# Optimization experiments

Measured on AMD Instinct MI355X. Metric: run time of the kernel, lower is better.

## Reference

```python
import jax, jax.numpy as jnp
import numpy as np

N_AGENTS = 512
HID = 256
OBS = 128


def setup_inputs() -> dict:
    key = jax.random.key(0)
    ks = jax.random.split(key, 10)
    s = 0.02  # weight init scale
    f32 = jnp.float32
    return {
        "inputs": jax.random.normal(ks[0], (N_AGENTS, OBS), f32),
        "fc1_w": jax.random.normal(ks[1], (HID, OBS), f32) * s,
        "fc1_b": jnp.zeros((HID,), f32),
        "in_proj_w": jax.random.normal(ks[2], (3 * HID, HID), f32) * s,
        "in_proj_b": jnp.zeros((3 * HID,), f32),
        "out_proj_w": jax.random.normal(ks[3], (HID, HID), f32) * s,
        "out_proj_b": jnp.zeros((HID,), f32),
        "fc2_w": jax.random.normal(ks[4], (HID, 2 * HID), f32) * s,
        "fc2_b": jnp.zeros((HID,), f32),
        "fc3_w": jax.random.normal(ks[5], (2, HID), f32) * s,
        "fc3_b": jnp.zeros((2,), f32),
        "vfc2_w": jax.random.normal(ks[6], (HID, HID * N_AGENTS), f32) * s,
        "vfc2_b": jnp.zeros((HID,), f32),
        "vfc3_w": jax.random.normal(ks[7], (1, HID), f32) * s,
        "vfc3_b": jnp.zeros((1,), f32),
    }


def reference(inputs, fc1_w, fc1_b, in_proj_w, in_proj_b, out_proj_w, out_proj_b,
              fc2_w, fc2_b, fc3_w, fc3_b, vfc2_w, vfc2_b, vfc3_w, vfc3_b):
    n = inputs.shape[0]
    d = fc1_w.shape[0]
    # per-agent embed
    hid = jax.nn.relu(inputs @ fc1_w.T + fc1_b)                 # [n, d]
    # single-head self-attention (torch MultiheadAttention, 1 head)
    qkv = hid @ in_proj_w.T + in_proj_b                         # [n, 3d]
    q, k, v = jnp.split(qkv, 3, axis=-1)
    scores = (q @ k.T) / jnp.sqrt(jnp.asarray(d, hid.dtype))    # [n, n]
    attn = jax.nn.softmax(scores, axis=-1)
    h = (attn @ v) @ out_proj_w.T + out_proj_b                  # [n, d]
    # all-pairs edge features restricted to strict upper triangle
    iu0, iu1 = jnp.triu_indices(n, 1)                           # P = n(n-1)/2
    pairs = jnp.concatenate([h[iu0], h[iu1]], axis=1)           # [P, 2d]
    x = jax.nn.relu(pairs @ fc2_w.T + fc2_b)                    # [P, d]
    action_out = jax.nn.softmax(x @ fc3_w.T + fc3_b, axis=-1)   # [P, 2]
    # value head over flattened node embeddings
    vh = jax.nn.relu(hid.reshape(1, -1) @ vfc2_w.T + vfc2_b)    # [1, d]
    value = vh @ vfc3_w.T + vfc3_b                              # [1, 1]
    value = jnp.broadcast_to(value, (action_out.shape[0], 1))   # [P, 1]
    return jnp.concatenate([action_out, value], axis=1)         # [P, 3]
```

## Files before the change

### kernel.cpp

```cpp
#include <hip/hip_runtime.h>
#include <math.h>

#define N_AG   512
#define HIDD   256
#define OBSD   128

__device__ __forceinline__ void fma4(float4& acc, float4 a, float4 b){
    acc.x += a.x*b.x; acc.y += a.y*b.y; acc.z += a.z*b.z; acc.w += a.w*b.w;
}
__device__ __forceinline__ float hsum(float4 a){ return (a.x+a.y)+(a.z+a.w); }

__device__ __forceinline__ void stage_rows(float* dst, const float* __restrict__ src,
        int row0, int stride, int colbase, int t){
    #pragma unroll
    for (int half = 0; half < 2; ++half){
        int idx = half*256 + t;
        int row = idx >> 3, c4 = idx & 7;
        float4 v = *(const float4*)(src + (row0+row)*stride + colbase + c4*4);
        dst[(c4*4+0)*68 + row] = v.x;
        dst[(c4*4+1)*68 + row] = v.y;
        dst[(c4*4+2)*68 + row] = v.z;
        dst[(c4*4+3)*68 + row] = v.w;
    }
}
__device__ __forceinline__ void tile_compute(const float* As, const float* Bs,
        int tx, int ty, float4 acc[4]){
    #pragma unroll
    for (int kk = 0; kk < 32; ++kk){
        float4 a = *(const float4*)(As + kk*68 + ty*4);
        float4 b = *(const float4*)(Bs + kk*68 + tx*4);
        acc[0].x += a.x*b.x; acc[0].y += a.x*b.y; acc[0].z += a.x*b.z; acc[0].w += a.x*b.w;
        acc[1].x += a.y*b.x; acc[1].y += a.y*b.y; acc[1].z += a.y*b.z; acc[1].w += a.y*b.w;
        acc[2].x += a.z*b.x; acc[2].y += a.z*b.y; acc[2].z += a.z*b.z; acc[2].w += a.z*b.w;
        acc[3].x += a.w*b.x; acc[3].y += a.w*b.y; acc[3].z += a.w*b.z; acc[3].w += a.w*b.w;
    }
}

__global__ __launch_bounds__(256, 2) void k_fc1(const float* __restrict__ in,
        const float* __restrict__ w, const float* __restrict__ b,
        float* __restrict__ hid){
    __shared__ float lin[8*OBSD];
    int at = blockIdx.y, ot = blockIdx.x, t = threadIdx.x;
    ((float4*)lin)[t] = ((const float4*)(in + at*8*OBSD))[t];
    __syncthreads();
    int ol = t & 63, g = t >> 6;
    int o = ot*64 + ol;
    const float4* w4 = (const float4*)(w + o*OBSD);
    const float4* la = (const float4*)(lin + (g*2)*OBSD);
    const float4* lb = (const float4*)(lin + (g*2+1)*OBSD);
    float4 a0 = {0,0,0,0}, a1 = {0,0,0,0};
    #pragma unroll
    for (int c = 0; c < OBSD/4; ++c){
        float4 wv = w4[c];
        fma4(a0, la[c], wv);
        fma4(a1, lb[c], wv);
    }
    float bb = b[o];
    int ag = at*8 + g*2;
    hid[ag*HIDD + o]     = fmaxf(hsum(a0) + bb, 0.f);
    hid[(ag+1)*HIDD + o] = fmaxf(hsum(a1) + bb, 0.f);
}

__global__ __launch_bounds__(256, 2) void k_qkv(const float* __restrict__ hid,
        const float* __restrict__ w, const float* __restrict__ b,
        float* __restrict__ qkv){
    __shared__ float lin[8*HIDD];
    int at = blockIdx.y, ot = blockIdx.x, t = threadIdx.x;
    const float4* in4 = (const float4*)(hid + at*8*HIDD);
    ((float4*)lin)[t]       = in4[t];
    ((float4*)lin)[t + 256] = in4[t + 256];
    __syncthreads();
    int ol = t & 63, g = t >> 6;
    int o = ot*64 + ol;
    const float4* w4 = (const float4*)(w + o*HIDD);
    const float4* la = (const float4*)(lin + (g*2)*HIDD);
    const float4* lb = (const float4*)(lin + (g*2+1)*HIDD);
    float4 a0 = {0,0,0,0}, a1 = {0,0,0,0};
    #pragma unroll 8
    for (int c = 0; c < HIDD/4; ++c){
        float4 wv = w4[c];
        fma4(a0, la[c], wv);
        fma4(a1, lb[c], wv);
    }
    float bb = b[o];
    int ag = at*8 + g*2;
    qkv[ag*768 + o]     = hsum(a0) + bb;
    qkv[(ag+1)*768 + o] = hsum(a1) + bb;
}

__global__ __launch_bounds__(256, 2) void k_big(const float* __restrict__ qkv,
        const float* __restrict__ ow, const float* __restrict__ hid,
        const float* __restrict__ vw_w, float* __restrict__ S,
        float* __restrict__ VW, float* __restrict__ partial){
    __shared__ float As[32*68];
    __shared__ float Bs[32*68];
    int t = threadIdx.x;
    int bid = blockIdx.x;
    if (bid < 64){
        int ti = bid >> 3, tj = bid & 7;
        int i0 = ti*64, j0 = tj*64;
        int tx = t & 15, ty = t >> 4;
        float4 acc[4] = {{0,0,0,0},{0,0,0,0},{0,0,0,0},{0,0,0,0}};
        for (int k0 = 0; k0 < 256; k0 += 32){
            __syncthreads();
            stage_rows(As, qkv, i0, 768, k0,       t);
            stage_rows(Bs, qkv, j0, 768, 256 + k0, t);
            __syncthreads();
            tile_compute(As, Bs, tx, ty, acc);
        }
        #pragma unroll
        for (int r = 0; r < 4; ++r){
            float4 o;
            o.x = acc[r].x*0.0625f; o.y = acc[r].y*0.0625f;
            o.z = acc[r].z*0.0625f; o.w = acc[r].w*0.0625f;
            *(float4*)(S + (i0+ty*4+r)*512 + j0 + tx*4) = o;
        }
        return;
    }
    if (bid < 96){
        int b2 = bid - 64;
        int ti = b2 >> 2, tj = b2 & 3;
        int j0 = ti*64, d0 = tj*64;
        int tx = t & 15, ty = t >> 4;
        float4 acc[4] = {{0,0,0,0},{0,0,0,0},{0,0,0,0},{0,0,0,0}};
        for (int k0 = 0; k0 < 256; k0 += 32){
            __syncthreads();
            stage_rows(As, qkv, j0, 768, 512 + k0, t);
            stage_rows(Bs, ow,  d0, 256, k0,       t);
            __syncthreads();
            tile_compute(As, Bs, tx, ty, acc);
        }
        #pragma unroll
        for (int r = 0; r < 4; ++r)
            *(float4*)(VW + (j0+ty*4+r)*256 + d0 + tx*4) = acc[r];
        return;
    }
    int id = bid - 96;
    int chunk = id & 7, o = id >> 3;
    const float4* h4 = (const float4*)hid;
    const float4* w4 = (const float4*)vw_w;
    long base  = (long)chunk*4096;
    long wbase = (long)o*32768 + base;
    float4 aa = {0,0,0,0}, ab = {0,0,0,0};
    #pragma unroll 4
    for (int it = 0; it < 8; ++it){
        fma4(aa, h4[base + it*256 + t],     w4[wbase + it*256 + t]);
        fma4(ab, h4[base + (it+8)*256 + t], w4[wbase + (it+8)*256 + t]);
    }
    float acc = hsum(aa) + hsum(ab);
    for (int off = 32; off; off >>= 1) acc += __shfl_xor(acc, off);
    int lane = t & 63, wid = t >> 6;
    if (lane == 0) As[wid] = acc;
    __syncthreads();
    if (t == 0) partial[o*8 + chunk] = As[0]+As[1]+As[2]+As[3];
}

__global__ __launch_bounds__(256, 2) void k_softmax(float* __restrict__ S){
    int t = threadIdx.x, w = t >> 6, ln = t & 63;
    float* row = S + (blockIdx.x*4 + w)*512;
    float v[8];
    float m = -1e30f;
    #pragma unroll
    for (int k = 0; k < 8; ++k){ v[k] = row[ln + k*64]; m = fmaxf(m, v[k]); }
    for (int off = 32; off; off >>= 1) m = fmaxf(m, __shfl_xor(m, off));
    float s = 0.f;
    #pragma unroll
    for (int k = 0; k < 8; ++k){ v[k] = expf(v[k] - m); s += v[k]; }
    for (int off = 32; off; off >>= 1) s += __shfl_xor(s, off);
    float inv = 1.f / s;
    #pragma unroll
    for (int k = 0; k < 8; ++k) row[ln + k*64] = v[k]*inv;
}

__global__ __launch_bounds__(256, 2) void k_h(const float* __restrict__ P,
        const float* __restrict__ VW, const float* __restrict__ ob,
        float* __restrict__ hout){
    __shared__ float As[32*68];
    __shared__ float Bs[32*68];
    int bid = blockIdx.x;
    int ti = bid >> 2, tj = bid & 3;
    int i0 = ti*64, d0 = tj*64;
    int t = threadIdx.x, tx = t & 15, ty = t >> 4;
    float4 acc[4] = {{0,0,0,0},{0,0,0,0},{0,0,0,0},{0,0,0,0}};
    for (int k0 = 0; k0 < 512; k0 += 32){
        __syncthreads();
        stage_rows(As, P, i0, 512, k0, t);
        #pragma unroll
        for (int half = 0; half < 2; ++half){
            int idx = half*256 + t;
            int kkr = idx >> 4, c4 = idx & 15;
            *(float4*)(Bs + kkr*68 + c4*4) = *(const float4*)(VW + (k0+kkr)*256 + d0 + c4*4);
        }
        __syncthreads();
        tile_compute(As, Bs, tx, ty, acc);
    }
    float4 bb = *(const float4*)(ob + d0 + tx*4);
    #pragma unroll
    for (int r = 0; r < 4; ++r){
        float4 o;
        o.x = acc[r].x + bb.x; o.y = acc[r].y + bb.y;
        o.z = acc[r].z + bb.z; o.w = acc[r].w + bb.w;
        *(float4*)(hout + (i0+ty*4+r)*256 + d0 + tx*4) = o;
    }
}

__global__ __launch_bounds__(256, 2) void k_ab_value(const float* __restrict__ hin,
        const float* __restrict__ w2, const float* __restrict__ b2,
        const float* __restrict__ partial, const float* __restrict__ vb,
        const float* __restrict__ v3w, const float* __restrict__ v3b,
        float* __restrict__ A, float* __restrict__ B, float* __restrict__ value){
    int t = threadIdx.x;
    if (blockIdx.x == 512){
        float s = vb[t];
        #pragma unroll
        for (int c = 0; c < 8; ++c) s += partial[t*8 + c];
        s = fmaxf(s, 0.f) * v3w[t];
        for (int off = 32; off; off >>= 1) s += __shfl_xor(s, off);
        __shared__ float redv[4];
        int lane = t & 63, wid = t >> 6;
        if (lane == 0) redv[wid] = s;
        __syncthreads();
        if (t == 0) value[0] = redv[0]+redv[1]+redv[2]+redv[3] + v3b[0];
        return;
    }
    __shared__ float lin[8*HIDD];
    int id = blockIdx.x, at = id >> 3, ot = id & 7;
    const float4* in4 = (const float4*)(hin + at*8*HIDD);
    ((float4*)lin)[t]       = in4[t];
    ((float4*)lin)[t + 256] = in4[t + 256];
    __syncthreads();
    int ol = t & 63, g = t >> 6;
    int o2 = ot*64 + ol;
    bool isA = o2 < HIDD;
    int o = isA ? o2 : o2 - HIDD;
    const float4* w4 = (const float4*)(w2 + o*512 + (isA ? 0 : HIDD));
    const float4* la = (const float4*)(lin + (g*2)*HIDD);
    const float4* lb = (const float4*)(lin + (g*2+1)*HIDD);
    float4 acc0 = {0,0,0,0}, acc1 = {0,0,0,0};
    #pragma unroll 8
    for (int c = 0; c < HIDD/4; ++c){
        float4 wv = w4[c];
        fma4(acc0, la[c], wv);
        fma4(acc1, lb[c], wv);
    }
    int a0 = at*8 + g*2;
    float* dst = isA ? A : B;
    float bb = isA ? b2[o] : 0.f;
    dst[a0*HIDD + o]     = hsum(acc0) + bb;
    dst[(a0+1)*HIDD + o] = hsum(acc1) + bb;
}

__global__ __launch_bounds__(256, 2) void k_pairs(const float* __restrict__ A,
        const float* __restrict__ B, const float* __restrict__ w3,
        const float* __restrict__ b3, const float* __restrict__ value,
        float* __restrict__ out){
    int ti = blockIdx.x, tj = blockIdx.y;
    if (tj < ti) return;
    __shared__ float la[16*260], lb[16*260], lw[256];
    int t = threadIdx.x;
    #pragma unroll
    for (int l = 0; l < 4; ++l){
        int idx = l*256 + t;
        int r = idx >> 6, c4 = idx & 63;
        ((float4*)la)[r*65 + c4] = ((const float4*)A)[(ti*16 + r)*64 + c4];
        ((float4*)lb)[r*65 + c4] = ((const float4*)B)[(tj*16 + r)*64 + c4];
    }
    lw[t] = w3[t] - w3[256 + t];
    __syncthreads();
    float val = value[0];
    float bd  = b3[0] - b3[1];
    int il = t >> 4, jl = t & 15;
    int i = ti*16 + il, j = tj*16 + jl;
    if (j > i){
        const float4* a4 = (const float4*)(la + il*260);
        const float4* b4 = (const float4*)(lb + jl*260);
        const float4* w4 = (const float4*)lw;
        float4 acc = {0,0,0,0};
        #pragma unroll 8
        for (int c = 0; c < 64; ++c){
            float4 aa = a4[c], bb = b4[c], wv = w4[c];
            acc.x += fmaxf(aa.x + bb.x, 0.f)*wv.x;
            acc.y += fmaxf(aa.y + bb.y, 0.f)*wv.y;
            acc.z += fmaxf(aa.z + bb.z, 0.f)*wv.z;
            acc.w += fmaxf(aa.w + bb.w, 0.f)*wv.w;
        }
        float z = hsum(acc) + bd;
        float o0 = 1.f/(1.f + expf(-z));
        int p = i*511 - (i*(i-1))/2 + (j - i - 1);
        out[3*p]   = o0;
        out[3*p+1] = 1.f - o0;
        out[3*p+2] = val;
    }
}

extern "C" void kernel_launch(void* const* d_in, const int* in_sizes, int n_in,
                              void* d_out, int out_size, void* d_ws, size_t ws_size,
                              hipStream_t stream){
    const float* inputs = (const float*)d_in[0];
    const float* fc1_w  = (const float*)d_in[1];
    const float* fc1_b  = (const float*)d_in[2];
    const float* inp_w  = (const float*)d_in[3];
    const float* inp_b  = (const float*)d_in[4];
    const float* outp_w = (const float*)d_in[5];
    const float* outp_b = (const float*)d_in[6];
    const float* fc2_w  = (const float*)d_in[7];
    const float* fc2_b  = (const float*)d_in[8];
    const float* fc3_w  = (const float*)d_in[9];
    const float* fc3_b  = (const float*)d_in[10];
    const float* vfc2_w = (const float*)d_in[11];
    const float* vfc2_b = (const float*)d_in[12];
    const float* vfc3_w = (const float*)d_in[13];
    const float* vfc3_b = (const float*)d_in[14];
    float* out = (float*)d_out;
    float* ws  = (float*)d_ws;
    float* hid     = ws;
    float* qkv     = ws + 131072;
    float* S       = ws + 524288;
    float* VW      = ws + 786432;
    float* h       = ws + 917504;
    float* A       = ws + 1048576;
    float* B       = ws + 1179648;
    float* partial = ws + 1310720;
    float* value   = ws + 1312768;

    k_fc1     <<<dim3(4, 64),  256, 0, stream>>>(inputs, fc1_w, fc1_b, hid);
    k_qkv     <<<dim3(12, 64), 256, 0, stream>>>(hid, inp_w, inp_b, qkv);
    k_big     <<<dim3(2144),   256, 0, stream>>>(qkv, outp_w, hid, vfc2_w, S, VW, partial);
    k_softmax <<<dim3(128),    256, 0, stream>>>(S);
    k_h       <<<dim3(32),     256, 0, stream>>>(S, VW, outp_b, h);
    k_ab_value<<<dim3(513),    256, 0, stream>>>(h, fc2_w, fc2_b, partial, vfc2_b, vfc3_w, vfc3_b, A, B, value);
    k_pairs   <<<dim3(32, 32), 256, 0, stream>>>(A, B, fc3_w, fc3_b, value, out);
}
```

Before: 299.0 us.

## Fuse pipeline into persistent megakernel with software grid barriers

Replaces the seven kernel launches with one persistent 512-block kernel whose stages are separated by atomic grid barriers. The large value-head weight stream is split across two stages so it runs alongside the attention GEMMs. Softmax is folded into the attn@V tile load, and fc1 and qkv are fused per agent group. The aim is to remove launch gaps and idle tails between small kernels, at the cost of barrier spin overhead and relying on all 512 blocks being co-resident for the barrier to avoid deadlock.

```diff
diff --git a/kernel.cpp b/kernel.cpp
--- a/kernel.cpp
+++ b/kernel.cpp
@@ -5,10 +5,30 @@
 #define HIDD   256
 #define OBSD   128
 
+#define NBLK   512u
+
 __device__ __forceinline__ void fma4(float4& acc, float4 a, float4 b){
     acc.x += a.x*b.x; acc.y += a.y*b.y; acc.z += a.z*b.z; acc.w += a.w*b.w;
 }
 __device__ __forceinline__ float hsum(float4 a){ return (a.x+a.y)+(a.z+a.w); }
+
+__device__ __forceinline__ void grid_barrier(unsigned* bar, unsigned* gen){
+    __threadfence();
+    __syncthreads();
+    if (threadIdx.x == 0){
+        unsigned g = __hip_atomic_load(gen, __ATOMIC_RELAXED, __HIP_MEMORY_SCOPE_AGENT);
+        unsigned a = __hip_atomic_fetch_add(bar, 1u, __ATOMIC_ACQ_REL, __HIP_MEMORY_SCOPE_AGENT) + 1u;
+        if (a == NBLK){
+            __hip_atomic_store(bar, 0u, __ATOMIC_RELAXED, __HIP_MEMORY_SCOPE_AGENT);
+            __hip_atomic_fetch_add(gen, 1u, __ATOMIC_RELEASE, __HIP_MEMORY_SCOPE_AGENT);
+        } else {
+            while (__hip_atomic_load(gen, __ATOMIC_ACQUIRE, __HIP_MEMORY_SCOPE_AGENT) == g)
+                __builtin_amdgcn_s_sleep(1);
+        }
+    }
+    __syncthreads();
+    __threadfence();
+}
 
 __device__ __forceinline__ void stage_rows(float* dst, const float* __restrict__ src,
         int row0, int stride, int colbase, int t){
@@ -36,109 +56,12 @@
     }
 }
 
-__global__ __launch_bounds__(256, 2) void k_fc1(const float* __restrict__ in,
-        const float* __restrict__ w, const float* __restrict__ b,
-        float* __restrict__ hid){
-    __shared__ float lin[8*OBSD];
-    int at = blockIdx.y, ot = blockIdx.x, t = threadIdx.x;
-    ((float4*)lin)[t] = ((const float4*)(in + at*8*OBSD))[t];
-    __syncthreads();
-    int ol = t & 63, g = t >> 6;
-    int o = ot*64 + ol;
-    const float4* w4 = (const float4*)(w + o*OBSD);
-    const float4* la = (const float4*)(lin + (g*2)*OBSD);
-    const float4* lb = (const float4*)(lin + (g*2+1)*OBSD);
-    float4 a0 = {0,0,0,0}, a1 = {0,0,0,0};
-    #pragma unroll
-    for (int c = 0; c < OBSD/4; ++c){
-        float4 wv = w4[c];
-        fma4(a0, la[c], wv);
-        fma4(a1, lb[c], wv);
-    }
-    float bb = b[o];
-    int ag = at*8 + g*2;
-    hid[ag*HIDD + o]     = fmaxf(hsum(a0) + bb, 0.f);
-    hid[(ag+1)*HIDD + o] = fmaxf(hsum(a1) + bb, 0.f);
-}
-
-__global__ __launch_bounds__(256, 2) void k_qkv(const float* __restrict__ hid,
-        const float* __restrict__ w, const float* __restrict__ b,
-        float* __restrict__ qkv){
-    __shared__ float lin[8*HIDD];
-    int at = blockIdx.y, ot = blockIdx.x, t = threadIdx.x;
-    const float4* in4 = (const float4*)(hid + at*8*HIDD);
-    ((float4*)lin)[t]       = in4[t];
-    ((float4*)lin)[t + 256] = in4[t + 256];
-    __syncthreads();
-    int ol = t & 63, g = t >> 6;
-    int o = ot*64 + ol;
-    const float4* w4 = (const float4*)(w + o*HIDD);
-    const float4* la = (const float4*)(lin + (g*2)*HIDD);
-    const float4* lb = (const float4*)(lin + (g*2+1)*HIDD);
-    float4 a0 = {0,0,0,0}, a1 = {0,0,0,0};
-    #pragma unroll 8
-    for (int c = 0; c < HIDD/4; ++c){
-        float4 wv = w4[c];
-        fma4(a0, la[c], wv);
-        fma4(a1, lb[c], wv);
-    }
-    float bb = b[o];
-    int ag = at*8 + g*2;
-    qkv[ag*768 + o]     = hsum(a0) + bb;
-    qkv[(ag+1)*768 + o] = hsum(a1) + bb;
-}
-
-__global__ __launch_bounds__(256, 2) void k_big(const float* __restrict__ qkv,
-        const float* __restrict__ ow, const float* __restrict__ hid,
-        const float* __restrict__ vw_w, float* __restrict__ S,
-        float* __restrict__ VW, float* __restrict__ partial){
-    __shared__ float As[32*68];
-    __shared__ float Bs[32*68];
-    int t = threadIdx.x;
-    int bid = blockIdx.x;
-    if (bid < 64){
-        int ti = bid >> 3, tj = bid & 7;
-        int i0 = ti*64, j0 = tj*64;
-        int tx = t & 15, ty = t >> 4;
-        float4 acc[4] = {{0,0,0,0},{0,0,0,0},{0,0,0,0},{0,0,0,0}};
-        for (int k0 = 0; k0 < 256; k0 += 32){
-            __syncthreads();
-            stage_rows(As, qkv, i0, 768, k0,       t);
-            stage_rows(Bs, qkv, j0, 768, 256 + k0, t);
-            __syncthreads();
-            tile_compute(As, Bs, tx, ty, acc);
-        }
-        #pragma unroll
-        for (int r = 0; r < 4; ++r){
-            float4 o;
-            o.x = acc[r].x*0.0625f; o.y = acc[r].y*0.0625f;
-            o.z = acc[r].z*0.0625f; o.w = acc[r].w*0.0625f;
-            *(float4*)(S + (i0+ty*4+r)*512 + j0 + tx*4) = o;
-        }
-        return;
-    }
-    if (bid < 96){
-        int b2 = bid - 64;
-        int ti = b2 >> 2, tj = b2 & 3;
-        int j0 = ti*64, d0 = tj*64;
-        int tx = t & 15, ty = t >> 4;
-        float4 acc[4] = {{0,0,0,0},{0,0,0,0},{0,0,0,0},{0,0,0,0}};
-        for (int k0 = 0; k0 < 256; k0 += 32){
-            __syncthreads();
-            stage_rows(As, qkv, j0, 768, 512 + k0, t);
-            stage_rows(Bs, ow,  d0, 256, k0,       t);
-            __syncthreads();
-            tile_compute(As, Bs, tx, ty, acc);
-        }
-        #pragma unroll
-        for (int r = 0; r < 4; ++r)
-            *(float4*)(VW + (j0+ty*4+r)*256 + d0 + tx*4) = acc[r];
-        return;
-    }
-    int id = bid - 96;
-    int chunk = id & 7, o = id >> 3;
+__device__ __forceinline__ void stream_unit(int u, const float* __restrict__ hid,
+        const float* __restrict__ vw2, float* __restrict__ partial,
+        float* red, int t){
+    int chunk = u & 7, o = u >> 3;
     const float4* h4 = (const float4*)hid;
-    const float4* w4 = (const float4*)vw_w;
+    const float4* w4 = (const float4*)vw2;
     long base  = (long)chunk*4096;
     long wbase = (long)o*32768 + base;
     float4 aa = {0,0,0,0}, ab = {0,0,0,0};
@@ -150,146 +73,276 @@
     float acc = hsum(aa) + hsum(ab);
     for (int off = 32; off; off >>= 1) acc += __shfl_xor(acc, off);
     int lane = t & 63, wid = t >> 6;
-    if (lane == 0) As[wid] = acc;
+    if (lane == 0) red[wid] = acc;
     __syncthreads();
-    if (t == 0) partial[o*8 + chunk] = As[0]+As[1]+As[2]+As[3];
-}
-
-__global__ __launch_bounds__(256, 2) void k_softmax(float* __restrict__ S){
-    int t = threadIdx.x, w = t >> 6, ln = t & 63;
-    float* row = S + (blockIdx.x*4 + w)*512;
-    float v[8];
-    float m = -1e30f;
-    #pragma unroll
-    for (int k = 0; k < 8; ++k){ v[k] = row[ln + k*64]; m = fmaxf(m, v[k]); }
-    for (int off = 32; off; off >>= 1) m = fmaxf(m, __shfl_xor(m, off));
-    float s = 0.f;
-    #pragma unroll
-    for (int k = 0; k < 8; ++k){ v[k] = expf(v[k] - m); s += v[k]; }
-    for (int off = 32; off; off >>= 1) s += __shfl_xor(s, off);
-    float inv = 1.f / s;
-    #pragma unroll
-    for (int k = 0; k < 8; ++k) row[ln + k*64] = v[k]*inv;
-}
-
-__global__ __launch_bounds__(256, 2) void k_h(const float* __restrict__ P,
-        const float* __restrict__ VW, const float* __restrict__ ob,
-        float* __restrict__ hout){
-    __shared__ float As[32*68];
-    __shared__ float Bs[32*68];
-    int bid = blockIdx.x;
-    int ti = bid >> 2, tj = bid & 3;
-    int i0 = ti*64, d0 = tj*64;
-    int t = threadIdx.x, tx = t & 15, ty = t >> 4;
-    float4 acc[4] = {{0,0,0,0},{0,0,0,0},{0,0,0,0},{0,0,0,0}};
-    for (int k0 = 0; k0 < 512; k0 += 32){
+    if (t == 0) partial[o*8 + chunk] = red[0]+red[1]+red[2]+red[3];
+}
+
+__global__ __launch_bounds__(256, 2) void k_mega(
+        const float* __restrict__ in,
+        const float* __restrict__ fc1w, const float* __restrict__ fc1b,
+        const float* __restrict__ ipw,  const float* __restrict__ ipb,
+        const float* __restrict__ opw,  const float* __restrict__ opb,
+        const float* __restrict__ fc2w, const float* __restrict__ fc2b,
+        const float* __restrict__ fc3w, const float* __restrict__ fc3b,
+        const float* __restrict__ vw2,  const float* __restrict__ vb2,
+        const float* __restrict__ vw3,  const float* __restrict__ vb3,
+        float* __restrict__ hid, float* __restrict__ qkv, float* __restrict__ S,
+        float* __restrict__ VW, float* __restrict__ h,
+        float* __restrict__ A, float* __restrict__ B,
+        float* __restrict__ partial, float* __restrict__ value,
+        float* __restrict__ out, unsigned* __restrict__ bar, unsigned* __restrict__ gen)
+{
+    __shared__ float smem[8704];
+    int bid = blockIdx.x, t = threadIdx.x;
+
+    {
+        int grp = bid >> 2, quarter = bid & 3;
+        int a0 = grp*4;
+        float* lin  = smem;
+        float* hidL = smem + 512;
+        if (t < 128) ((float4*)lin)[t] = ((const float4*)(in + a0*OBSD))[t];
         __syncthreads();
-        stage_rows(As, P, i0, 512, k0, t);
+        {
+            int o = t;
+            const float4* w4 = (const float4*)(fc1w + o*OBSD);
+            const float4* l4 = (const float4*)lin;
+            float4 acc[4] = {{0,0,0,0},{0,0,0,0},{0,0,0,0},{0,0,0,0}};
+            #pragma unroll
+            for (int c = 0; c < OBSD/4; ++c){
+                float4 wv = w4[c];
+                #pragma unroll
+                for (int g = 0; g < 4; ++g) fma4(acc[g], l4[g*32 + c], wv);
+            }
+            float bb = fc1b[o];
+            #pragma unroll
+            for (int g = 0; g < 4; ++g){
+                float v = fmaxf(hsum(acc[g]) + bb, 0.f);
+                hidL[g*HIDD + o] = v;
+                if (quarter == 0) hid[(a0+g)*HIDD + o] = v;
+            }
+        }
+        __syncthreads();
+        const float4* hl4 = (const float4*)hidL;
         #pragma unroll
-        for (int half = 0; half < 2; ++half){
-            int idx = half*256 + t;
-            int kkr = idx >> 4, c4 = idx & 15;
-            *(float4*)(Bs + kkr*68 + c4*4) = *(const float4*)(VW + (k0+kkr)*256 + d0 + c4*4);
-        }
+        for (int r = 0; r < 3; ++r){
+            int idx = r*256 + t;
+            int g = idx / 192, oo = idx - g*192;
+            int o = quarter*192 + oo;
+            const float4* w4 = (const float4*)(ipw + o*HIDD);
+            float4 acc = {0,0,0,0};
+            #pragma unroll 8
+            for (int c = 0; c < HIDD/4; ++c) fma4(acc, hl4[g*64 + c], w4[c]);
+            qkv[(a0+g)*768 + o] = hsum(acc) + ipb[o];
+        }
+    }
+    grid_barrier(bar, gen);
+
+    {
+        float* As = smem;
+        float* Bs = smem + 2176;
+        if (bid < 64){
+            int ti = bid >> 3, tj = bid & 7;
+            int i0 = ti*64, j0 = tj*64;
+            int tx = t & 15, ty = t >> 4;
+            float4 acc[4] = {{0,0,0,0},{0,0,0,0},{0,0,0,0},{0,0,0,0}};
+            for (int k0 = 0; k0 < 256; k0 += 32){
+                __syncthreads();
+                stage_rows(As, qkv, i0, 768, k0,       t);
+                stage_rows(Bs, qkv, j0, 768, 256 + k0, t);
+                __syncthreads();
+                tile_compute(As, Bs, tx, ty, acc);
+            }
+            #pragma unroll
+            for (int r = 0; r < 4; ++r){
+                float4 o;
+                o.x = acc[r].x*0.0625f; o.y = acc[r].y*0.0625f;
+                o.z = acc[r].z*0.0625f; o.w = acc[r].w*0.0625f;
+                *(float4*)(S + (i0+ty*4+r)*512 + j0 + tx*4) = o;
+            }
+        } else if (bid < 96){
+            int b2 = bid - 64;
+            int ti = b2 >> 2, tj = b2 & 3;
+            int j0 = ti*64, d0 = tj*64;
+            int tx = t & 15, ty = t >> 4;
+            float4 acc[4] = {{0,0,0,0},{0,0,0,0},{0,0,0,0},{0,0,0,0}};
+            for (int k0 = 0; k0 < 256; k0 += 32){
+                __syncthreads();
+                stage_rows(As, qkv, j0, 768, 512 + k0, t);
+                stage_rows(Bs, opw, d0, 256, k0,       t);
+                __syncthreads();
+                tile_compute(As, Bs, tx, ty, acc);
+            }
+            #pragma unroll
+            for (int r = 0; r < 4; ++r)
+                *(float4*)(VW + (j0+ty*4+r)*256 + d0 + tx*4) = acc[r];
+        } else {
+            for (int u = bid - 96; u < 1024; u += 416){
+                __syncthreads();
+                stream_unit(u, hid, vw2, partial, smem + 4352, t);
+            }
+        }
+    }
+    grid_barrier(bar, gen);
+
+    {
+        if (bid < 64){
+            int ti = bid >> 2, tj = bid & 3;
+            int i0 = ti*32, d0 = tj*64;
+            float* As   = smem;
+            float* Bs   = smem + 2176;
+            float* rowm = smem + 4352;
+            float* rowi = smem + 4384;
+            {
+                int r = t >> 3, c8 = t & 7;
+                const float4* Sr = (const float4*)(S + (i0 + r)*512);
+                float m = -1e30f;
+                #pragma unroll
+                for (int k = 0; k < 16; ++k){
+                    float4 v = Sr[c8 + k*8];
+                    m = fmaxf(m, fmaxf(fmaxf(v.x, v.y), fmaxf(v.z, v.w)));
+                }
+                m = fmaxf(m, __shfl_xor(m, 1));
+                m = fmaxf(m, __shfl_xor(m, 2));
+                m = fmaxf(m, __shfl_xor(m, 4));
+                float s = 0.f;
+                #pragma unroll
+                for (int k = 0; k < 16; ++k){
+                    float4 v = Sr[c8 + k*8];
+                    s += expf(v.x-m) + expf(v.y-m) + expf(v.z-m) + expf(v.w-m);
+                }
+                s += __shfl_xor(s, 1); s += __shfl_xor(s, 2); s += __shfl_xor(s, 4);
+                if (c8 == 0){ rowm[r] = m; rowi[r] = 1.f/s; }
+            }
+            __syncthreads();
+            int tx = t & 15, ty = t >> 4;
+            float4 acc0 = {0,0,0,0}, acc1 = {0,0,0,0};
+            for (int k0 = 0; k0 < 512; k0 += 32){
+                __syncthreads();
+                {
+                    int row = t >> 3, c4 = t & 7;
+                    float m = rowm[row], iv = rowi[row];
+                    float4 v = *(const float4*)(S + (i0+row)*512 + k0 + c4*4);
+                    As[(c4*4+0)*68 + row] = expf(v.x - m)*iv;
+                    As[(c4*4+1)*68 + row] = expf(v.y - m)*iv;
+                    As[(c4*4+2)*68 + row] = expf(v.z - m)*iv;
+                    As[(c4*4+3)*68 + row] = expf(v.w - m)*iv;
+                }
+                #pragma unroll
+                for (int half = 0; half < 2; ++half){
+                    int idx = half*256 + t;
+                    int kkr = idx >> 4, c4 = idx & 15;
+                    *(float4*)(Bs + kkr*68 + c4*4) = *(const float4*)(VW + (k0+kkr)*256 + d0 + c4*4);
+                }
+                __syncthreads();
+                #pragma unroll
+                for (int kk = 0; kk < 32; ++kk){
+                    float2 a = *(const float2*)(As + kk*68 + ty*2);
+                    float4 b = *(const float4*)(Bs + kk*68 + tx*4);
+                    acc0.x += a.x*b.x; acc0.y += a.x*b.y; acc0.z += a.x*b.z; acc0.w += a.x*b.w;
+                    acc1.x += a.y*b.x; acc1.y += a.y*b.y; acc1.z += a.y*b.z; acc1.w += a.y*b.w;
+                }
+            }
+            float4 bb = *(const float4*)(opb + d0 + tx*4);
+            float4 o0, o1;
+            o0.x = acc0.x+bb.x; o0.y = acc0.y+bb.y; o0.z = acc0.z+bb.z; o0.w = acc0.w+bb.w;
+            o1.x = acc1.x+bb.x; o1.y = acc1.y+bb.y; o1.z = acc1.z+bb.z; o1.w = acc1.w+bb.w;
+            *(float4*)(h + (i0+ty*2  )*256 + d0 + tx*4) = o0;
+            *(float4*)(h + (i0+ty*2+1)*256 + d0 + tx*4) = o1;
+        } else {
+            for (int u = 1024 + (bid - 64); u < 2048; u += 448){
+                __syncthreads();
+                stream_unit(u, hid, vw2, partial, smem + 4352, t);
+            }
+        }
+    }
+    grid_barrier(bar, gen);
+
+    {
+        float* lin  = smem;
+        float* redv = smem + 2048;
+        if (bid == 511){
+            float s = vb2[t];
+            #pragma unroll
+            for (int c = 0; c < 8; ++c) s += partial[t*8 + c];
+            s = fmaxf(s, 0.f) * vw3[t];
+            for (int off = 32; off; off >>= 1) s += __shfl_xor(s, off);
+            int lane = t & 63, wid = t >> 6;
+            if (lane == 0) redv[wid] = s;
+            __syncthreads();
+            if (t == 0) value[0] = redv[0]+redv[1]+redv[2]+redv[3] + vb3[0];
+            __syncthreads();
+        }
+        int at = bid >> 3, ot = bid & 7;
+        const float4* in4 = (const float4*)(h + at*8*HIDD);
+        ((float4*)lin)[t]       = in4[t];
+        ((float4*)lin)[t + 256] = in4[t + 256];
         __syncthreads();
-        tile_compute(As, Bs, tx, ty, acc);
-    }
-    float4 bb = *(const float4*)(ob + d0 + tx*4);
-    #pragma unroll
-    for (int r = 0; r < 4; ++r){
-        float4 o;
-        o.x = acc[r].x + bb.x; o.y = acc[r].y + bb.y;
-        o.z = acc[r].z + bb.z; o.w = acc[r].w + bb.w;
-        *(float4*)(hout + (i0+ty*4+r)*256 + d0 + tx*4) = o;
-    }
-}
-
-__global__ __launch_bounds__(256, 2) void k_ab_value(const float* __restrict__ hin,
-        const float* __restrict__ w2, const float* __restrict__ b2,
-        const float* __restrict__ partial, const float* __restrict__ vb,
-        const float* __restrict__ v3w, const float* __restrict__ v3b,
-        float* __restrict__ A, float* __restrict__ B, float* __restrict__ value){
-    int t = threadIdx.x;
-    if (blockIdx.x == 512){
-        float s = vb[t];
-        #pragma unroll
-        for (int c = 0; c < 8; ++c) s += partial[t*8 + c];
-        s = fmaxf(s, 0.f) * v3w[t];
-        for (int off = 32; off; off >>= 1) s += __shfl_xor(s, off);
-        __shared__ float redv[4];
-        int lane = t & 63, wid = t >> 6;
-        if (lane == 0) redv[wid] = s;
-        __syncthreads();
-        if (t == 0) value[0] = redv[0]+redv[1]+redv[2]+redv[3] + v3b[0];
-        return;
-    }
-    __shared__ float lin[8*HIDD];
-    int id = blockIdx.x, at = id >> 3, ot = id & 7;
-    const float4* in4 = (const float4*)(hin + at*8*HIDD);
-    ((float4*)lin)[t]       = in4[t];
-    ((float4*)lin)[t + 256] = in4[t + 256];
-    __syncthreads();
-    int ol = t & 63, g = t >> 6;
-    int o2 = ot*64 + ol;
-    bool isA = o2 < HIDD;
-    int o = isA ? o2 : o2 - HIDD;
-    const float4* w4 = (const float4*)(w2 + o*512 + (isA ? 0 : HIDD));
-    const float4* la = (const float4*)(lin + (g*2)*HIDD);
-    const float4* lb = (const float4*)(lin + (g*2+1)*HIDD);
-    float4 acc0 = {0,0,0,0}, acc1 = {0,0,0,0};
-    #pragma unroll 8
-    for (int c = 0; c < HIDD/4; ++c){
-        float4 wv = w4[c];
-        fma4(acc0, la[c], wv);
-        fma4(acc1, lb[c], wv);
-    }
-    int a0 = at*8 + g*2;
-    float* dst = isA ? A : B;
-    float bb = isA ? b2[o] : 0.f;
-    dst[a0*HIDD + o]     = hsum(acc0) + bb;
-    dst[(a0+1)*HIDD + o] = hsum(acc1) + bb;
-}
-
-__global__ __launch_bounds__(256, 2) void k_pairs(const float* __restrict__ A,
-        const float* __restrict__ B, const float* __restrict__ w3,
-        const float* __restrict__ b3, const float* __restrict__ value,
-        float* __restrict__ out){
-    int ti = blockIdx.x, tj = blockIdx.y;
-    if (tj < ti) return;
-    __shared__ float la[16*260], lb[16*260], lw[256];
-    int t = threadIdx.x;
-    #pragma unroll
-    for (int l = 0; l < 4; ++l){
-        int idx = l*256 + t;
-        int r = idx >> 6, c4 = idx & 63;
-        ((float4*)la)[r*65 + c4] = ((const float4*)A)[(ti*16 + r)*64 + c4];
-        ((float4*)lb)[r*65 + c4] = ((const float4*)B)[(tj*16 + r)*64 + c4];
-    }
-    lw[t] = w3[t] - w3[256 + t];
-    __syncthreads();
-    float val = value[0];
-    float bd  = b3[0] - b3[1];
-    int il = t >> 4, jl = t & 15;
-    int i = ti*16 + il, j = tj*16 + jl;
-    if (j > i){
-        const float4* a4 = (const float4*)(la + il*260);
-        const float4* b4 = (const float4*)(lb + jl*260);
-        const float4* w4 = (const float4*)lw;
-        float4 acc = {0,0,0,0};
+        int ol = t & 63, g = t >> 6;
+        int o2 = ot*64 + ol;
+        bool isA = o2 < HIDD;
+        int o = isA ? o2 : o2 - HIDD;
+        const float4* w4 = (const float4*)(fc2w + o*512 + (isA ? 0 : HIDD));
+        const float4* la4 = (const float4*)(lin + (g*2)*HIDD);
+        const float4* lb4 = (const float4*)(lin + (g*2+1)*HIDD);
+        float4 acc0 = {0,0,0,0}, acc1 = {0,0,0,0};
         #pragma unroll 8
-        for (int c = 0; c < 64; ++c){
-            float4 aa = a4[c], bb = b4[c], wv = w4[c];
-            acc.x += fmaxf(aa.x + bb.x, 0.f)*wv.x;
-            acc.y += fmaxf(aa.y + bb.y, 0.f)*wv.y;
-            acc.z += fmaxf(aa.z + bb.z, 0.f)*wv.z;
-            acc.w += fmaxf(aa.w + bb.w, 0.f)*wv.w;
-        }
-        float z = hsum(acc) + bd;
-        float o0 = 1.f/(1.f + expf(-z));
-        int p = i*511 - (i*(i-1))/2 + (j - i - 1);
-        out[3*p]   = o0;
-        out[3*p+1] = 1.f - o0;
-        out[3*p+2] = val;
+        for (int c = 0; c < HIDD/4; ++c){
+            float4 wv = w4[c];
+            fma4(acc0, la4[c], wv);
+            fma4(acc1, lb4[c], wv);
+        }
+        int a0 = at*8 + g*2;
+        float* dst = isA ? A : B;
+        float bb = isA ? fc2b[o] : 0.f;
+        dst[a0*HIDD + o]     = hsum(acc0) + bb;
+        dst[(a0+1)*HIDD + o] = hsum(acc1) + bb;
+    }
+    grid_barrier(bar, gen);
+
+    {
+        float* la = smem;
+        float* lb = smem + 4160;
+        float* lw = smem + 8320;
+        float val = value[0];
+        float bd  = fc3b[0] - fc3b[1];
+        for (int tile = bid; tile < 528; tile += 512){
+            int rem = tile, ti = 0;
+            while (rem >= 32 - ti){ rem -= 32 - ti; ++ti; }
+            int tj = ti + rem;
+            __syncthreads();
+            #pragma unroll
+            for (int l = 0; l < 4; ++l){
+                int idx = l*256 + t;
+                int r = idx >> 6, c4 = idx & 63;
+                ((float4*)la)[r*65 + c4] = ((const float4*)A)[(ti*16 + r)*64 + c4];
+                ((float4*)lb)[r*65 + c4] = ((const float4*)B)[(tj*16 + r)*64 + c4];
+            }
+            lw[t] = fc3w[t] - fc3w[256 + t];
+            __syncthreads();
+            int il = t >> 4, jl = t & 15;
+            int i = ti*16 + il, j = tj*16 + jl;
+            if (j > i){
+                const float4* a4 = (const float4*)(la + il*260);
+                const float4* b4 = (const float4*)(lb + jl*260);
+                const float4* w4 = (const float4*)lw;
+                float4 acc = {0,0,0,0};
+                #pragma unroll 8
+                for (int c = 0; c < 64; ++c){
+                    float4 aa = a4[c], bb = b4[c], wv = w4[c];
+                    acc.x += fmaxf(aa.x + bb.x, 0.f)*wv.x;
+                    acc.y += fmaxf(aa.y + bb.y, 0.f)*wv.y;
+                    acc.z += fmaxf(aa.z + bb.z, 0.f)*wv.z;
+                    acc.w += fmaxf(aa.w + bb.w, 0.f)*wv.w;
+                }
+                float z = hsum(acc) + bd;
+                float o0 = 1.f/(1.f + expf(-z));
+                int p = i*511 - (i*(i-1))/2 + (j - i - 1);
+                out[3*p]   = o0;
+                out[3*p+1] = 1.f - o0;
+                out[3*p+2] = val;
+            }
+        }
     }
 }
 
@@ -322,12 +375,13 @@
     float* B       = ws + 1179648;
     float* partial = ws + 1310720;
     float* value   = ws + 1312768;
-
-    k_fc1     <<<dim3(4, 64),  256, 0, stream>>>(inputs, fc1_w, fc1_b, hid);
-    k_qkv     <<<dim3(12, 64), 256, 0, stream>>>(hid, inp_w, inp_b, qkv);
-    k_big     <<<dim3(2144),   256, 0, stream>>>(qkv, outp_w, hid, vfc2_w, S, VW, partial);
-    k_softmax <<<dim3(128),    256, 0, stream>>>(S);
-    k_h       <<<dim3(32),     256, 0, stream>>>(S, VW, outp_b, h);
-    k_ab_value<<<dim3(513),    256, 0, stream>>>(h, fc2_w, fc2_b, partial, vfc2_b, vfc3_w, vfc3_b, A, B, value);
-    k_pairs   <<<dim3(32, 32), 256, 0, stream>>>(A, B, fc3_w, fc3_b, value, out);
-}
+    unsigned* bar  = (unsigned*)(ws + 1312772);
+    unsigned* gen  = bar + 1;
+
+    hipMemsetAsync(bar, 0, 8, stream);
+
+    k_mega<<<dim3(512), dim3(256), 0, stream>>>(
+        inputs, fc1_w, fc1_b, inp_w, inp_b, outp_w, outp_b,
+        fc2_w, fc2_b, fc3_w, fc3_b, vfc2_w, vfc2_b, vfc3_w, vfc3_b,
+        hid, qkv, S, VW, h, A, B, partial, value, out, bar, gen);
+}
```

Result: slower. 959.2 us (+220.8%).
